# Performance work log

Hardware: AMD Instinct MI355X
Metric: run time of the kernel (lower is better)

Reference implementation:

```python
import jax, jax.numpy as jnp
import numpy as np

D_MODEL = 1024
N_HEADS = 16
HEAD_DIM = D_MODEL // N_HEADS
NUM_SINK = 4
WINDOW = 512
B, S = 1, 4096


def _sink_visible(S):
    # visible[i, j] = (j <= i) & ((j < NUM_SINK) | (j >= i - WINDOW + 1))
    i = jnp.arange(S)[:, None]
    j = jnp.arange(S)[None, :]
    return (j <= i) & ((j < NUM_SINK) | (j >= i - WINDOW + 1))


def setup_inputs() -> dict:
    key = jax.random.key(0)
    kx, kq, kk, kv, ko = jax.random.split(key, 5)
    sc = 1.0 / np.sqrt(D_MODEL)
    return {
        "x": jax.random.normal(kx, (B, S, D_MODEL), dtype=jnp.float32),
        "Wq": jax.random.normal(kq, (D_MODEL, D_MODEL), dtype=jnp.float32) * sc,
        "Wk": jax.random.normal(kk, (D_MODEL, D_MODEL), dtype=jnp.float32) * sc,
        "Wv": jax.random.normal(kv, (D_MODEL, D_MODEL), dtype=jnp.float32) * sc,
        "Wo": jax.random.normal(ko, (D_MODEL, D_MODEL), dtype=jnp.float32) * sc,
    }


def reference(x, Wq, Wk, Wv, Wo):
    Bx, Sx, D = x.shape
    H, hd = N_HEADS, HEAD_DIM
    # nn.Linear (no bias): y = x @ W^T
    q = (x @ Wq.T).reshape(Bx, Sx, H, hd).transpose(0, 2, 1, 3)  # (B,H,S,hd)
    k = (x @ Wk.T).reshape(Bx, Sx, H, hd).transpose(0, 2, 1, 3)
    v = (x @ Wv.T).reshape(Bx, Sx, H, hd).transpose(0, 2, 1, 3)
    scale = 1.0 / np.sqrt(hd)
    scores = jnp.einsum("bhqd,bhkd->bhqk", q, k) * scale  # (B,H,S,S)
    visible = _sink_visible(Sx)  # (S,S) bool; every row has j=i visible
    scores = jnp.where(visible[None, None], scores, -jnp.inf)
    attn = jax.nn.softmax(scores, axis=-1)
    out = jnp.einsum("bhqk,bhkd->bhqd", attn, v)
    out = out.transpose(0, 2, 1, 3).reshape(Bx, Sx, D)
    return out @ Wo.T
```

## Files before the change

kernel.cpp:

```cpp
#include <hip/hip_runtime.h>
#include <stdint.h>

#define AS1 __attribute__((address_space(1)))
#define AS3 __attribute__((address_space(3)))

typedef short short8 __attribute__((ext_vector_type(8)));
typedef unsigned short ushort8 __attribute__((ext_vector_type(8)));
typedef __bf16 bf16x8 __attribute__((ext_vector_type(8)));
typedef float floatx4 __attribute__((ext_vector_type(4)));

__device__ __forceinline__ floatx4 mfma16(short8 a, short8 b, floatx4 c) {
  return __builtin_amdgcn_mfma_f32_16x16x32_bf16(
      __builtin_bit_cast(bf16x8, a), __builtin_bit_cast(bf16x8, b), c, 0, 0, 0);
}

__device__ __forceinline__ unsigned short f2bf(float f) {
  uint32_t u = __builtin_bit_cast(uint32_t, f);
  u = (u + 0x7FFFu + ((u >> 16) & 1u)) >> 16;
  return (unsigned short)u;
}

__device__ __forceinline__ uint32_t cvt_pk_bf16(float a, float b) {
  uint32_t d;
  asm("v_cvt_pk_bf16_f32 %0, %1, %2" : "=v"(d) : "v"(a), "v"(b));
  return d;
}

__global__ __launch_bounds__(256) void convert_pack(
    const float4* __restrict__ x, const float4* __restrict__ wq,
    const float4* __restrict__ wk, const float4* __restrict__ wv,
    const float4* __restrict__ wo, ushort4* __restrict__ xb,
    ushort4* __restrict__ wqkvb, ushort4* __restrict__ wob) {
  int i = blockIdx.x * 256 + threadIdx.x;
  const float4* src;
  ushort4* dst;
  if (i < (1 << 20)) {
    src = x + i;
    dst = xb + i;
  } else {
    int t = i - (1 << 20);
    int r = t >> 18;
    int j = t & ((1 << 18) - 1);
    src = (r == 0 ? wq : r == 1 ? wk : r == 2 ? wv : wo) + j;
    dst = (r < 3) ? (wqkvb + (r << 18) + j) : (wob + j);
  }
  float4 v = *src;
  ushort4 o;
  o.x = f2bf(v.x);
  o.y = f2bf(v.y);
  o.z = f2bf(v.z);
  o.w = f2bf(v.w);
  *dst = o;
}

template <typename OutT>
__global__ __launch_bounds__(256) void gemm_bt(const unsigned short* __restrict__ A,
                                               const unsigned short* __restrict__ Bm,
                                               OutT* __restrict__ C, int N, int K) {
  __shared__ unsigned short lds[32 * 512];
  const int tid = threadIdx.x;
  const int lane = tid & 63;
  const int w = tid >> 6;
  const int wr = w >> 1, wc = w & 1;
  const int tm = blockIdx.x * 128, tn = blockIdx.y * 128;
  const int lrow = lane & 15;
  const int lk = (lane >> 4) * 8;

  floatx4 acc[4][4];
#pragma unroll
  for (int i = 0; i < 4; ++i)
#pragma unroll
    for (int j = 0; j < 4; ++j) acc[i][j] = floatx4{0.f, 0.f, 0.f, 0.f};

  for (int k0 = 0; k0 < K; k0 += 64) {
#pragma unroll
    for (int c = w; c < 32; c += 4) {
      const unsigned short* g;
      if (c < 16) {
        int mt = c >> 1, ks = c & 1;
        g = A + (size_t)(tm + mt * 16 + lrow) * K + (k0 + ks * 32 + lk);
      } else {
        int cc = c - 16;
        int nt = cc >> 1, ks = cc & 1;
        g = Bm + (size_t)(tn + nt * 16 + lrow) * K + (k0 + ks * 32 + lk);
      }
      __builtin_amdgcn_global_load_lds((const AS1 uint32_t*)g,
                                       (AS3 uint32_t*)(&lds[c * 512]), 16, 0, 0);
    }
    __syncthreads();
#pragma unroll
    for (int ks = 0; ks < 2; ++ks) {
      short8 af[4], bf[4];
#pragma unroll
      for (int i = 0; i < 4; ++i)
        af[i] = *(const short8*)&lds[((wr * 4 + i) * 2 + ks) * 512 + lane * 8];
#pragma unroll
      for (int j = 0; j < 4; ++j)
        bf[j] = *(const short8*)&lds[(16 + (wc * 4 + j) * 2 + ks) * 512 + lane * 8];
#pragma unroll
      for (int i = 0; i < 4; ++i)
#pragma unroll
        for (int j = 0; j < 4; ++j) acc[i][j] = mfma16(af[i], bf[j], acc[i][j]);
    }
    __syncthreads();
  }
  const int r0 = (lane >> 4) * 4;
#pragma unroll
  for (int i = 0; i < 4; ++i)
#pragma unroll
    for (int j = 0; j < 4; ++j)
#pragma unroll
      for (int r = 0; r < 4; ++r) {
        int row = tm + wr * 64 + i * 16 + r0 + r;
        int col = tn + wc * 64 + j * 16 + lrow;
        float v = acc[i][j][r];
        if constexpr (sizeof(OutT) == 2)
          C[(size_t)row * N + col] = f2bf(v);
        else
          C[(size_t)row * N + col] = v;
      }
}

__global__ __launch_bounds__(256) void gemm64(const unsigned short* __restrict__ A,
                                              const unsigned short* __restrict__ Bm,
                                              float* __restrict__ C, int N, int K) {
  __shared__ unsigned short lds[24 * 512];
  const int tid = threadIdx.x;
  const int lane = tid & 63;
  const int w = tid >> 6;
  const int wr = w >> 1, wc = w & 1;
  const int tm = blockIdx.x * 64, tn = blockIdx.y * 128;
  const int lrow = lane & 15;
  const int lk = (lane >> 4) * 8;

  floatx4 acc[2][4];
#pragma unroll
  for (int i = 0; i < 2; ++i)
#pragma unroll
    for (int j = 0; j < 4; ++j) acc[i][j] = floatx4{0.f, 0.f, 0.f, 0.f};

  for (int k0 = 0; k0 < K; k0 += 64) {
#pragma unroll
    for (int c = w * 6; c < w * 6 + 6; ++c) {
      const unsigned short* g;
      if (c < 8) {
        int mt = c >> 1, ks = c & 1;
        g = A + (size_t)(tm + mt * 16 + lrow) * K + (k0 + ks * 32 + lk);
      } else {
        int cc = c - 8;
        int nt = cc >> 1, ks = cc & 1;
        g = Bm + (size_t)(tn + nt * 16 + lrow) * K + (k0 + ks * 32 + lk);
      }
      __builtin_amdgcn_global_load_lds((const AS1 uint32_t*)g,
                                       (AS3 uint32_t*)(&lds[c * 512]), 16, 0, 0);
    }
    __syncthreads();
#pragma unroll
    for (int ks = 0; ks < 2; ++ks) {
      short8 af[2], bf[4];
#pragma unroll
      for (int i = 0; i < 2; ++i)
        af[i] = *(const short8*)&lds[((wr * 2 + i) * 2 + ks) * 512 + lane * 8];
#pragma unroll
      for (int j = 0; j < 4; ++j)
        bf[j] = *(const short8*)&lds[(8 + (wc * 4 + j) * 2 + ks) * 512 + lane * 8];
#pragma unroll
      for (int i = 0; i < 2; ++i)
#pragma unroll
        for (int j = 0; j < 4; ++j) acc[i][j] = mfma16(af[i], bf[j], acc[i][j]);
    }
    __syncthreads();
  }
  const int r0 = (lane >> 4) * 4;
#pragma unroll
  for (int i = 0; i < 2; ++i)
#pragma unroll
    for (int j = 0; j < 4; ++j)
#pragma unroll
      for (int r = 0; r < 4; ++r) {
        int row = tm + (wr * 2 + i) * 16 + r0 + r;
        int col = tn + (wc * 4 + j) * 16 + lrow;
        C[(size_t)row * N + col] = acc[i][j][r];
      }
}

__global__ __launch_bounds__(256) void attn_kernel(const unsigned short* __restrict__ qkv,
                                                   unsigned short* __restrict__ aout) {
  __shared__ unsigned short Klds[2][16 * 512];
  __shared__ unsigned short VT[64 * 136];
  __shared__ unsigned short PT[4][16 * 136];

  const int tid = threadIdx.x;
  const int lane = tid & 63;
  const int w = tid >> 6;
  const int lrow = lane & 15;
  const int lkg = lane >> 4;

  const int i = blockIdx.x;
  const int half = i >> 8;
  const int j = (i >> 3) & 31;
  const int h = 2 * (i & 7) + half;
  const int qb = half ? (31 - j) : j;
  const int q0 = qb * 128;

  short8 qf[2][2];
#pragma unroll
  for (int qt = 0; qt < 2; ++qt)
#pragma unroll
    for (int ks = 0; ks < 2; ++ks)
      qf[qt][ks] = *(const short8*)&qkv[(size_t)(q0 + qt * 64 + w * 16 + lrow) * 3072 +
                                        h * 64 + ks * 32 + lkg * 8];

  float m_i[2], l_i[2];
  floatx4 o[4][2];
#pragma unroll
  for (int qt = 0; qt < 2; ++qt) {
    m_i[qt] = -1e30f;
    l_i[qt] = 0.f;
#pragma unroll
    for (int nt = 0; nt < 4; ++nt) o[nt][qt] = floatx4{0.f, 0.f, 0.f, 0.f};
  }

  const float scale2 = 0.125f * 1.44269504088896f;

  if (w < 2) {
    const unsigned short* g = &qkv[(size_t)lrow * 3072 + 1024 + h * 64 + w * 32 + lkg * 8];
    __builtin_amdgcn_global_load_lds((const AS1 uint32_t*)g,
                                     (AS3 uint32_t*)(&Klds[0][w * 512]), 16, 0, 0);
  }
  {
    if (lane < 16) {
      const unsigned short* g0 = &qkv[(size_t)(2 * lane) * 3072 + 2048 + h * 64 + w * 16];
      ushort8 a0 = *(const ushort8*)g0;
      ushort8 a1 = *(const ushort8*)(g0 + 8);
      ushort8 b0 = *(const ushort8*)(g0 + 3072);
      ushort8 b1 = *(const ushort8*)(g0 + 3080);
      uint32_t* vt = (uint32_t*)VT;
#pragma unroll
      for (int dd = 0; dd < 8; ++dd) {
        vt[(w * 16 + dd) * 68 + lane] = (uint32_t)a0[dd] | ((uint32_t)b0[dd] << 16);
        vt[(w * 16 + 8 + dd) * 68 + lane] = (uint32_t)a1[dd] | ((uint32_t)b1[dd] << 16);
      }
    }
  }
  const int kb0 = (q0 - 511 < 16) ? 16 : (q0 - 511);
#pragma unroll
  for (int c = 0; c < 4; ++c) {
    int ch = w * 4 + c;
    int kt = ch >> 1, ks = ch & 1;
    const unsigned short* g =
        &qkv[(size_t)(kb0 + kt * 16 + lrow) * 3072 + 1024 + h * 64 + ks * 32 + lkg * 8];
    __builtin_amdgcn_global_load_lds((const AS1 uint32_t*)g,
                                     (AS3 uint32_t*)(&Klds[1][ch * 512]), 16, 0, 0);
  }
  ushort8 va0, va1, vb0, vb1;
  {
    const unsigned short* g0 = &qkv[(size_t)(kb0 + 2 * lane) * 3072 + 2048 + h * 64 + w * 16];
    va0 = *(const ushort8*)g0;
    va1 = *(const ushort8*)(g0 + 8);
    vb0 = *(const ushort8*)(g0 + 3072);
    vb1 = *(const ushort8*)(g0 + 3080);
  }
  __syncthreads();

#pragma unroll
  for (int qt = 0; qt < 2; ++qt) {
    const int qq = q0 + qt * 64 + w * 16 + lrow;
    floatx4 s0 = floatx4{0.f, 0.f, 0.f, 0.f};
#pragma unroll
    for (int ks = 0; ks < 2; ++ks) {
      short8 kf = *(const short8*)&Klds[0][ks * 512 + lane * 8];
      s0 = mfma16(kf, qf[qt][ks], s0);
    }
    float mx = -1e30f;
    float sv[4];
#pragma unroll
    for (int r = 0; r < 4; ++r) {
      int key = lkg * 4 + r;
      bool vis = (key <= qq) && ((key < 4) || (key >= qq - 511));
      sv[r] = vis ? s0[r] * scale2 : -1e30f;
      mx = fmaxf(mx, sv[r]);
    }
    mx = fmaxf(mx, __shfl_xor(mx, 16));
    mx = fmaxf(mx, __shfl_xor(mx, 32));
    m_i[qt] = mx;
    float p0 = exp2f(sv[0] - mx), p1 = exp2f(sv[1] - mx);
    float p2 = exp2f(sv[2] - mx), p3 = exp2f(sv[3] - mx);
    float ps = (p0 + p1) + (p2 + p3);
    *(uint2*)&PT[w][lrow * 136 + lkg * 4] = uint2{cvt_pk_bf16(p0, p1), cvt_pk_bf16(p2, p3)};
    *(uint2*)&PT[w][lrow * 136 + 16 + lkg * 4] = uint2{0u, 0u};
    ps += __shfl_xor(ps, 16);
    ps += __shfl_xor(ps, 32);
    l_i[qt] = ps;
    short8 pf = *(const short8*)&PT[w][lrow * 136 + lkg * 8];
#pragma unroll
    for (int nt = 0; nt < 4; ++nt) {
      short8 vf = *(const short8*)&VT[(nt * 16 + lrow) * 136 + lkg * 8];
      o[nt][qt] = mfma16(vf, pf, o[nt][qt]);
    }
  }

  int nbuf = 1;
  for (int kb = kb0; kb < q0 + 128; kb += 128) {
    const bool hasnext = (kb + 128 < q0 + 128);
    __syncthreads();
    {
      uint32_t* vt = (uint32_t*)VT;
#pragma unroll
      for (int dd = 0; dd < 8; ++dd) {
        vt[(w * 16 + dd) * 68 + lane] = (uint32_t)va0[dd] | ((uint32_t)vb0[dd] << 16);
        vt[(w * 16 + 8 + dd) * 68 + lane] = (uint32_t)va1[dd] | ((uint32_t)vb1[dd] << 16);
      }
    }
    __syncthreads();

    if (hasnext) {
      const int kn = kb + 128;
#pragma unroll
      for (int c = 0; c < 4; ++c) {
        int ch = w * 4 + c;
        int kt = ch >> 1, ks = ch & 1;
        const unsigned short* g =
            &qkv[(size_t)(kn + kt * 16 + lrow) * 3072 + 1024 + h * 64 + ks * 32 + lkg * 8];
        __builtin_amdgcn_global_load_lds((const AS1 uint32_t*)g,
                                         (AS3 uint32_t*)(&Klds[1 - nbuf][ch * 512]), 16, 0, 0);
      }
      const unsigned short* g0 = &qkv[(size_t)(kn + 2 * lane) * 3072 + 2048 + h * 64 + w * 16];
      va0 = *(const ushort8*)g0;
      va1 = *(const ushort8*)(g0 + 8);
      vb0 = *(const ushort8*)(g0 + 3072);
      vb1 = *(const ushort8*)(g0 + 3080);
    }

#pragma unroll
    for (int qt = 0; qt < 2; ++qt) {
      const int qaT = q0 + qt * 64 + w * 16;
      const int qq = qaT + lrow;
      floatx4 s[8];
#pragma unroll
      for (int ct = 0; ct < 8; ++ct) {
        s[ct] = floatx4{0.f, 0.f, 0.f, 0.f};
#pragma unroll
        for (int ks = 0; ks < 2; ++ks) {
          short8 kf = *(const short8*)&Klds[nbuf][(ct * 2 + ks) * 512 + lane * 8];
          s[ct] = mfma16(kf, qf[qt][ks], s[ct]);
        }
      }
      const bool full = (kb + 127 <= qaT) && (kb >= qaT + 15 - 511);
      float mx = -1e30f;
#pragma unroll
      for (int ct = 0; ct < 8; ++ct)
#pragma unroll
        for (int r = 0; r < 4; ++r) {
          float val = s[ct][r] * scale2;
          if (!full) {
            int key = kb + ct * 16 + lkg * 4 + r;
            bool vis = (key <= qq) && (key >= qq - 511);
            val = vis ? val : -1e30f;
          }
          s[ct][r] = val;
          mx = fmaxf(mx, val);
        }
      mx = fmaxf(mx, __shfl_xor(mx, 16));
      mx = fmaxf(mx, __shfl_xor(mx, 32));
      float nm = fmaxf(m_i[qt], mx);
      float alpha = exp2f(m_i[qt] - nm);
      m_i[qt] = nm;

      float ps = 0.f;
#pragma unroll
      for (int ct = 0; ct < 8; ++ct) {
        float p0 = exp2f(s[ct][0] - nm), p1 = exp2f(s[ct][1] - nm);
        float p2 = exp2f(s[ct][2] - nm), p3 = exp2f(s[ct][3] - nm);
        ps += (p0 + p1) + (p2 + p3);
        *(uint2*)&PT[w][lrow * 136 + ct * 16 + lkg * 4] =
            uint2{cvt_pk_bf16(p0, p1), cvt_pk_bf16(p2, p3)};
      }
      ps += __shfl_xor(ps, 16);
      ps += __shfl_xor(ps, 32);
      l_i[qt] = l_i[qt] * alpha + ps;

#pragma unroll
      for (int nt = 0; nt < 4; ++nt)
#pragma unroll
        for (int r = 0; r < 4; ++r) o[nt][qt][r] *= alpha;

#pragma unroll
      for (int kk = 0; kk < 4; ++kk) {
        short8 pf = *(const short8*)&PT[w][lrow * 136 + kk * 32 + lkg * 8];
#pragma unroll
        for (int nt = 0; nt < 4; ++nt) {
          short8 vf = *(const short8*)&VT[(nt * 16 + lrow) * 136 + kk * 32 + lkg * 8];
          o[nt][qt] = mfma16(vf, pf, o[nt][qt]);
        }
      }
    }
    nbuf ^= 1;
  }

#pragma unroll
  for (int qt = 0; qt < 2; ++qt) {
    const int qq = q0 + qt * 64 + w * 16 + lrow;
    const float inv = 1.0f / l_i[qt];
#pragma unroll
    for (int nt = 0; nt < 4; ++nt) {
      floatx4 ov = o[nt][qt];
      uint32_t lo = cvt_pk_bf16(ov[0] * inv, ov[1] * inv);
      uint32_t hi = cvt_pk_bf16(ov[2] * inv, ov[3] * inv);
      *(uint2*)&aout[(size_t)qq * 1024 + h * 64 + nt * 16 + lkg * 4] = uint2{lo, hi};
    }
  }
}

extern "C" void kernel_launch(void* const* d_in, const int* in_sizes, int n_in,
                              void* d_out, int out_size, void* d_ws, size_t ws_size,
                              hipStream_t stream) {
  const float* x = (const float*)d_in[0];
  const float* wq = (const float*)d_in[1];
  const float* wk = (const float*)d_in[2];
  const float* wv = (const float*)d_in[3];
  const float* wo = (const float*)d_in[4];

  char* ws = (char*)d_ws;
  unsigned short* Xb = (unsigned short*)(ws);
  unsigned short* Wqkv = (unsigned short*)(ws + (8u << 20));
  unsigned short* Wob = (unsigned short*)(ws + (14u << 20));
  unsigned short* QKV = (unsigned short*)(ws + (16u << 20));
  unsigned short* AO = (unsigned short*)(ws + (40u << 20));

  convert_pack<<<8192, 256, 0, stream>>>((const float4*)x, (const float4*)wq,
                                         (const float4*)wk, (const float4*)wv,
                                         (const float4*)wo, (ushort4*)Xb,
                                         (ushort4*)Wqkv, (ushort4*)Wob);
  gemm_bt<unsigned short><<<dim3(32, 24), 256, 0, stream>>>(Xb, Wqkv, QKV, 3072, 1024);
  attn_kernel<<<512, 256, 0, stream>>>(QKV, AO);
  gemm64<<<dim3(64, 8), 256, 0, stream>>>(AO, Wob, (float*)d_out, 1024, 1024);
}
```

Measured before the change: 198.1 us.

## Double-buffer GEMM LDS staging and remap tiles for XCD locality

Both GEMM kernels now use two LDS buffers. The next K-slice's global-to-LDS loads are issued before the MFMAs on the current slice, so memory latency overlaps with compute. Block IDs are also remapped so blocks landing on the same XCD work on a compact group of output tiles, which improves L2 reuse. The remap hardcodes grid sizes (96 and 64 blocks per XCD), so it assumes the specific problem shape, and it doubles LDS use, which may lower occupancy.

```diff
diff --git a/kernel.cpp b/kernel.cpp
--- a/kernel.cpp
+++ b/kernel.cpp
@@ -57,12 +57,19 @@
 __global__ __launch_bounds__(256) void gemm_bt(const unsigned short* __restrict__ A,
                                                const unsigned short* __restrict__ Bm,
                                                OutT* __restrict__ C, int N, int K) {
-  __shared__ unsigned short lds[32 * 512];
+  __shared__ unsigned short lds[2][32 * 512];
   const int tid = threadIdx.x;
   const int lane = tid & 63;
   const int w = tid >> 6;
   const int wr = w >> 1, wc = w & 1;
-  const int tm = blockIdx.x * 128, tn = blockIdx.y * 128;
+
+  const int lid = blockIdx.y * gridDim.x + blockIdx.x;
+  const int xcd = lid & 7;
+  const int wgid = xcd * 96 + (lid >> 3);
+  const int s = wgid >> 5, w5 = wgid & 31;
+  const int mt = (s & 3) * 8 + (w5 & 7);
+  const int nt = (s >> 2) * 4 + (w5 >> 3);
+  const int tm = mt * 128, tn = nt * 128;
   const int lrow = lane & 15;
   const int lk = (lane >> 4) * 8;
 
@@ -72,31 +79,39 @@
 #pragma unroll
     for (int j = 0; j < 4; ++j) acc[i][j] = floatx4{0.f, 0.f, 0.f, 0.f};
 
-  for (int k0 = 0; k0 < K; k0 += 64) {
+  auto stage = [&](int buf, int k0) {
 #pragma unroll
     for (int c = w; c < 32; c += 4) {
       const unsigned short* g;
       if (c < 16) {
-        int mt = c >> 1, ks = c & 1;
-        g = A + (size_t)(tm + mt * 16 + lrow) * K + (k0 + ks * 32 + lk);
+        int mtt = c >> 1, ks = c & 1;
+        g = A + (size_t)(tm + mtt * 16 + lrow) * K + (k0 + ks * 32 + lk);
       } else {
         int cc = c - 16;
-        int nt = cc >> 1, ks = cc & 1;
-        g = Bm + (size_t)(tn + nt * 16 + lrow) * K + (k0 + ks * 32 + lk);
+        int ntt = cc >> 1, ks = cc & 1;
+        g = Bm + (size_t)(tn + ntt * 16 + lrow) * K + (k0 + ks * 32 + lk);
       }
       __builtin_amdgcn_global_load_lds((const AS1 uint32_t*)g,
-                                       (AS3 uint32_t*)(&lds[c * 512]), 16, 0, 0);
-    }
-    __syncthreads();
+                                       (AS3 uint32_t*)(&lds[buf][c * 512]), 16, 0, 0);
+    }
+  };
+
+  stage(0, 0);
+  __syncthreads();
+
+  const int T = K >> 6;
+  for (int t = 0; t < T; ++t) {
+    if (t + 1 < T) stage((t + 1) & 1, (t + 1) << 6);
+    const unsigned short* L = lds[t & 1];
 #pragma unroll
     for (int ks = 0; ks < 2; ++ks) {
       short8 af[4], bf[4];
 #pragma unroll
       for (int i = 0; i < 4; ++i)
-        af[i] = *(const short8*)&lds[((wr * 4 + i) * 2 + ks) * 512 + lane * 8];
+        af[i] = *(const short8*)&L[((wr * 4 + i) * 2 + ks) * 512 + lane * 8];
 #pragma unroll
       for (int j = 0; j < 4; ++j)
-        bf[j] = *(const short8*)&lds[(16 + (wc * 4 + j) * 2 + ks) * 512 + lane * 8];
+        bf[j] = *(const short8*)&L[(16 + (wc * 4 + j) * 2 + ks) * 512 + lane * 8];
 #pragma unroll
       for (int i = 0; i < 4; ++i)
 #pragma unroll
@@ -104,6 +119,7 @@
     }
     __syncthreads();
   }
+
   const int r0 = (lane >> 4) * 4;
 #pragma unroll
   for (int i = 0; i < 4; ++i)
@@ -124,12 +140,19 @@
 __global__ __launch_bounds__(256) void gemm64(const unsigned short* __restrict__ A,
                                               const unsigned short* __restrict__ Bm,
                                               float* __restrict__ C, int N, int K) {
-  __shared__ unsigned short lds[24 * 512];
+  __shared__ unsigned short lds[2][24 * 512];
   const int tid = threadIdx.x;
   const int lane = tid & 63;
   const int w = tid >> 6;
   const int wr = w >> 1, wc = w & 1;
-  const int tm = blockIdx.x * 64, tn = blockIdx.y * 128;
+
+  const int lid = blockIdx.y * gridDim.x + blockIdx.x;
+  const int xcd = lid & 7;
+  const int wgid = xcd * 64 + (lid >> 3);
+  const int s = wgid >> 5, w5 = wgid & 31;
+  const int mt = (s & 3) * 16 + (w5 & 15);
+  const int nt = (s >> 2) * 2 + (w5 >> 4);
+  const int tm = mt * 64, tn = nt * 128;
   const int lrow = lane & 15;
   const int lk = (lane >> 4) * 8;
 
@@ -139,31 +162,39 @@
 #pragma unroll
     for (int j = 0; j < 4; ++j) acc[i][j] = floatx4{0.f, 0.f, 0.f, 0.f};
 
-  for (int k0 = 0; k0 < K; k0 += 64) {
+  auto stage = [&](int buf, int k0) {
 #pragma unroll
     for (int c = w * 6; c < w * 6 + 6; ++c) {
       const unsigned short* g;
       if (c < 8) {
-        int mt = c >> 1, ks = c & 1;
-        g = A + (size_t)(tm + mt * 16 + lrow) * K + (k0 + ks * 32 + lk);
+        int mtt = c >> 1, ks = c & 1;
+        g = A + (size_t)(tm + mtt * 16 + lrow) * K + (k0 + ks * 32 + lk);
       } else {
         int cc = c - 8;
-        int nt = cc >> 1, ks = cc & 1;
-        g = Bm + (size_t)(tn + nt * 16 + lrow) * K + (k0 + ks * 32 + lk);
+        int ntt = cc >> 1, ks = cc & 1;
+        g = Bm + (size_t)(tn + ntt * 16 + lrow) * K + (k0 + ks * 32 + lk);
       }
       __builtin_amdgcn_global_load_lds((const AS1 uint32_t*)g,
-                                       (AS3 uint32_t*)(&lds[c * 512]), 16, 0, 0);
-    }
-    __syncthreads();
+                                       (AS3 uint32_t*)(&lds[buf][c * 512]), 16, 0, 0);
+    }
+  };
+
+  stage(0, 0);
+  __syncthreads();
+
+  const int T = K >> 6;
+  for (int t = 0; t < T; ++t) {
+    if (t + 1 < T) stage((t + 1) & 1, (t + 1) << 6);
+    const unsigned short* L = lds[t & 1];
 #pragma unroll
     for (int ks = 0; ks < 2; ++ks) {
       short8 af[2], bf[4];
 #pragma unroll
       for (int i = 0; i < 2; ++i)
-        af[i] = *(const short8*)&lds[((wr * 2 + i) * 2 + ks) * 512 + lane * 8];
+        af[i] = *(const short8*)&L[((wr * 2 + i) * 2 + ks) * 512 + lane * 8];
 #pragma unroll
       for (int j = 0; j < 4; ++j)
-        bf[j] = *(const short8*)&lds[(8 + (wc * 4 + j) * 2 + ks) * 512 + lane * 8];
+        bf[j] = *(const short8*)&L[(8 + (wc * 4 + j) * 2 + ks) * 512 + lane * 8];
 #pragma unroll
       for (int i = 0; i < 2; ++i)
 #pragma unroll
@@ -171,6 +202,7 @@
     }
     __syncthreads();
   }
+
   const int r0 = (lane >> 4) * 4;
 #pragma unroll
   for (int i = 0; i < 2; ++i)
```

Measured after the change: 202.9 us. 2.4% more time.
